# Performance work log

Hardware: AMD Instinct MI355X
Metric: run time of the kernel (lower is better)

## Reference

```python
import jax, jax.numpy as jnp
import numpy as np

K, N, E, D = 4, 2048, 4096, 128
BETA = 0.6
EPS = 0.01           # epsilon in hard-sigmoid gating
LAM = 0.05           # lambda_schedule
TC0, TCMAX = 0.3, 0.7
COS_EPS = 1e-8       # F.cosine_similarity eps
MAX_SCORED_EDGES = 500
EDGE_DENSITY = 0.008


def setup_inputs() -> dict:
    key = jax.random.key(0)
    ks = jax.random.split(key, 8)
    s = 0.02
    H = (jax.random.uniform(ks[0], (K, N, E)) < EDGE_DENSITY).astype(jnp.float32)
    X = jax.random.normal(ks[1], (N, D), jnp.float32)
    return dict(
        H=H, X=X, epoch=50,
        mlp_w1=jax.random.normal(ks[2], (K, D, D), jnp.float32) * s,
        mlp_b1=jnp.zeros((K, D), jnp.float32),
        mlp_w2=jax.random.normal(ks[3], (K, D, D), jnp.float32) * s,
        mlp_b2=jnp.zeros((K, D), jnp.float32),
        comp_W=jax.random.normal(ks[4], (K, D, D), jnp.float32) * 0.01,
        att_w1=jax.random.normal(ks[5], (K, D, D // 2), jnp.float32) * s,
        att_b1=jnp.zeros((K, D // 2), jnp.float32),
        att_w2=jax.random.normal(ks[6], (K, D // 2, 1), jnp.float32) * s,
        att_b2=jnp.zeros((K, 1), jnp.float32),
    )


def reference(H, X, epoch, mlp_w1, mlp_b1, mlp_w2, mlp_b2, comp_W,
              att_w1, att_b1, att_w2, att_b2):
    # ---- component level (Eq. 4, batched over K) ----
    h1 = jax.nn.relu(jnp.einsum('nd,kdh->knh', X, mlp_w1) + mlp_b1[:, None, :])
    Xk = jnp.einsum('knh,khe->kne', h1, mlp_w2) + mlp_b2[:, None, :]        # [K,N,D]
    a1 = jax.nn.relu(jnp.einsum('knd,kdh->knh', Xk, att_w1) + att_b1[:, None, :])
    att = jax.nn.sigmoid(jnp.einsum('knh,kho->kno', a1, att_w2) + att_b2[:, None, :])
    S_att = att.mean(axis=(1, 2))                                            # [K]
    frob = jnp.sqrt((comp_W ** 2).sum(axis=(1, 2)))                          # ||W_k||_F
    featn = jnp.sqrt((Xk ** 2).sum(axis=(1, 2)))                             # ||MLP(X_k)||_2 (Frobenius)
    imp = BETA * frob * featn + (1.0 - BETA) * S_att
    pi_c = jax.nn.softmax(imp)
    theta_c = TC0 + (1.0 - jnp.exp(-LAM * epoch)) * (TCMAX - TC0)            # Eq. 3 schedule
    gates = jnp.clip((pi_c - theta_c) / EPS + 0.5, 0.0, 1.0)                 # hard sigmoid
    # K_min = max(1, int(0.1*K)) = 1 -> force top-1 gate open
    keep = jax.nn.one_hot(jnp.argmax(gates), K, dtype=gates.dtype)
    gates = jnp.maximum(gates, keep)

    xnorm = jnp.linalg.norm(X, axis=1)                                       # [N]
    xhat = X / jnp.maximum(xnorm, COS_EPS)[:, None]
    er = jnp.arange(E)
    eye = jnp.eye(N, dtype=bool)

    Hp_l, eg_l, npi_l = [], [], []
    for k in range(K):  # small fixed component count
        Hk = H[k]
        mask = Hk > 0                                                        # [N,E]
        cnt = mask.sum(axis=0)                                               # nodes per hyperedge
        order = jnp.cumsum(mask, axis=0)
        i = jnp.argmax(mask, axis=0)                                         # first incident node
        j = jnp.argmax(mask & (order == 2), axis=0)                          # second incident node
        cos = (xhat[i] * xhat[j]).sum(-1)                                    # [E]
        A = Hk[i, er] * Hk[j, er]                                            # A_ij per edge
        # torch loop: only first 500 edges scored; <2-node edges get 0.1; rest 0
        imp_e = jnp.where(er < MAX_SCORED_EDGES,
                          jnp.where(cnt >= 2, A * cos, 0.1), 0.0)
        pi_e = jax.nn.softmax(imp_e)
        theta_e = jnp.minimum(theta_c, pi_e.mean() + jnp.std(pi_e, ddof=1))  # torch.std unbiased
        eg = jnp.clip((pi_e - theta_e) / EPS + 0.5, 0.0, 1.0)
        eg = jnp.where((eg.sum() < 1.0) & (er == jnp.argmax(pi_e)), 1.0, eg)
        eg_eff = jnp.where(gates[k] > 0.5, eg, jnp.ones_like(eg))
        Hp = Hk * gates[k] * eg_eff[None, :]                                 # pruned incidence

        # ---- node level (Eq. 7) on pruned graph ----
        B = (Hp > 0).astype(Hk.dtype)
        Adj = ((B @ B.T) > 0) & (~eye)                                       # shared-hyperedge neighbors
        degf = Adj.sum(axis=1).astype(Hk.dtype)
        nsum = Adj.astype(Hk.dtype) @ xhat                                   # sum of neighbor unit vecs
        avg = jnp.where(degf > 0, (xhat * nsum).sum(-1) / jnp.maximum(degf, 1.0), 0.0)
        npi = jax.nn.softmax(avg * xnorm)
        Hp_l.append(Hp); eg_l.append(eg); npi_l.append(npi)

    return (jnp.stack(Hp_l), gates, jnp.stack(eg_l), jnp.stack(npi_l))
```

## Files before the change

kernel.cpp:

```cpp
#include <hip/hip_runtime.h>
#include <math.h>

#define KCOMP 4
#define NN 2048
#define EE 4096
#define DD 128
#define MAXNE 96
#define MAXSE 500
#define BETA_C 0.6f
#define EPS_G 0.01f
#define LAM_S 0.05f
#define TC0_C 0.3f
#define TCMAX_C 0.7f
#define COS_EPS_C 1e-8f

typedef float vf4 __attribute__((ext_vector_type(4)));

static const size_t OFF_XHAT   = 0;
static const size_t OFF_XNORM  = 1048576;
static const size_t OFF_SCAL   = 1056768;
static const size_t OFF_NCNT   = 1057024;
static const size_t OFF_EMASK  = 1089792;
static const size_t OFF_NELIST = 5284096;
static const size_t OFF_IMPE   = 6856960;
static const size_t OFF_EGS    = 6865152;
static const size_t OFF_Z      = 6930688;
static const size_t OFF_FEAT   = 6963456;
static const size_t OFF_ATT    = 6965504;
static const size_t OFF_FROB   = 6967552;

__global__ __launch_bounds__(1024) void k_d1(
    const float4* __restrict__ H4, unsigned* __restrict__ emask,
    const float* __restrict__ X, float* __restrict__ xhat, float* __restrict__ xnorm,
    const float* __restrict__ w1, const float* __restrict__ b1,
    const float* __restrict__ w2, const float* __restrict__ b2,
    const float* __restrict__ aw1, const float* __restrict__ ab1,
    const float* __restrict__ aw2, const float* __restrict__ ab2,
    const float4* __restrict__ compW4,
    float* __restrict__ featA, float* __restrict__ attA, float* __restrict__ frobA) {
  __shared__ char smem[28928];
  int b = blockIdx.x, t = threadIdx.x;
  if (b < 256) {
    unsigned* lds = (unsigned*)smem;
    int k = b >> 6;
    int rem = b & 63;
    int ch_super = rem >> 4;
    int e4_super = rem & 15;
    int chi = t >> 6;
    int e4i = t & 63;
    int ch = ch_super * 16 + chi;
    int e4 = e4_super * 64 + e4i;
    int n0 = ch * 32;
    const float4* p = H4 + ((size_t)(k * NN + n0)) * (EE / 4) + e4;
    unsigned w0 = 0, w1b = 0, w2b = 0, w3 = 0;
    for (int rb = 0; rb < 32; rb += 8) {
      float4 v[8];
#pragma unroll
      for (int u = 0; u < 8; ++u) v[u] = p[(size_t)(rb + u) * (EE / 4)];
#pragma unroll
      for (int u = 0; u < 8; ++u) {
        unsigned bit = 1u << (rb + u);
        w0  |= (v[u].x > 0.f) ? bit : 0u;
        w1b |= (v[u].y > 0.f) ? bit : 0u;
        w2b |= (v[u].z > 0.f) ? bit : 0u;
        w3  |= (v[u].w > 0.f) ? bit : 0u;
      }
    }
    int el = e4i * 4;
    lds[(el + 0) * 17 + chi] = w0;
    lds[(el + 1) * 17 + chi] = w1b;
    lds[(el + 2) * 17 + chi] = w2b;
    lds[(el + 3) * 17 + chi] = w3;
    __syncthreads();
    int e_base = e4_super * 256;
    int wi = t & 15;
    int eo = t >> 4;
#pragma unroll
    for (int it = 0; it < 4; ++it) {
      int e_local = it * 64 + eo;
      emask[((size_t)(k * EE) + e_base + e_local) * 64 + ch_super * 16 + wi] =
          lds[e_local * 17 + wi];
    }
    return;
  }
  if (b < 384) {
    int node = (b - 256) * 16 + (t >> 6);
    int lane = t & 63;
    float2 v = ((const float2*)X)[(size_t)node * 64 + lane];
    float ss = v.x * v.x + v.y * v.y;
    for (int o = 32; o > 0; o >>= 1) ss += __shfl_xor(ss, o, 64);
    float nrm = sqrtf(ss);
    float den = fmaxf(nrm, COS_EPS_C);
    if (lane == 0) xnorm[node] = nrm;
    float2 o2; o2.x = v.x / den; o2.y = v.y / den;
    ((float2*)xhat)[(size_t)node * 64 + lane] = o2;
    return;
  }
  if (b < 896) {
    int mb = b - 384;
    int k = mb >> 7;
    int bx = mb & 127;
    float* Xs  = (float*)smem;
    float* H1s = Xs + 2048;
    float* XKs = H1s + 2048;
    float* A1s = XKs + 2048;
    float* red = A1s + 1024;
    int n0 = bx * 16;
    for (int i = t; i < 16 * 128; i += 1024) Xs[i] = X[(size_t)n0 * 128 + i];
    __syncthreads();

    int h = t & 127, g = t >> 7;
    const float* W1 = w1 + (size_t)k * 128 * 128;
    float acc0 = b1[k * 128 + h], acc1 = acc0;
    for (int d = 0; d < 128; d += 4) {
      float wa = W1[(d + 0) * 128 + h];
      float wb = W1[(d + 1) * 128 + h];
      float wc = W1[(d + 2) * 128 + h];
      float wd = W1[(d + 3) * 128 + h];
      float4 x0 = *(const float4*)&Xs[(g * 2 + 0) * 128 + d];
      float4 x1 = *(const float4*)&Xs[(g * 2 + 1) * 128 + d];
      acc0 = fmaf(x0.x, wa, acc0); acc0 = fmaf(x0.y, wb, acc0);
      acc0 = fmaf(x0.z, wc, acc0); acc0 = fmaf(x0.w, wd, acc0);
      acc1 = fmaf(x1.x, wa, acc1); acc1 = fmaf(x1.y, wb, acc1);
      acc1 = fmaf(x1.z, wc, acc1); acc1 = fmaf(x1.w, wd, acc1);
    }
    H1s[(g * 2 + 0) * 128 + h] = fmaxf(acc0, 0.f);
    H1s[(g * 2 + 1) * 128 + h] = fmaxf(acc1, 0.f);
    __syncthreads();

    const float* W2 = w2 + (size_t)k * 128 * 128;
    acc0 = b2[k * 128 + h]; acc1 = acc0;
    for (int d = 0; d < 128; d += 4) {
      float wa = W2[(d + 0) * 128 + h];
      float wb = W2[(d + 1) * 128 + h];
      float wc = W2[(d + 2) * 128 + h];
      float wd = W2[(d + 3) * 128 + h];
      float4 x0 = *(const float4*)&H1s[(g * 2 + 0) * 128 + d];
      float4 x1 = *(const float4*)&H1s[(g * 2 + 1) * 128 + d];
      acc0 = fmaf(x0.x, wa, acc0); acc0 = fmaf(x0.y, wb, acc0);
      acc0 = fmaf(x0.z, wc, acc0); acc0 = fmaf(x0.w, wd, acc0);
      acc1 = fmaf(x1.x, wa, acc1); acc1 = fmaf(x1.y, wb, acc1);
      acc1 = fmaf(x1.z, wc, acc1); acc1 = fmaf(x1.w, wd, acc1);
    }
    float fpart = fmaf(acc1, acc1, acc0 * acc0);
    XKs[(g * 2 + 0) * 128 + h] = acc0;
    XKs[(g * 2 + 1) * 128 + h] = acc1;
    __syncthreads();

    int h2 = t & 63, g4 = t >> 6;
    const float* AW1 = aw1 + (size_t)k * 128 * 64;
    float a0 = ab1[k * 64 + h2];
    for (int d = 0; d < 128; d += 4) {
      float4 xv = *(const float4*)&XKs[g4 * 128 + d];
      a0 = fmaf(xv.x, AW1[(d + 0) * 64 + h2], a0);
      a0 = fmaf(xv.y, AW1[(d + 1) * 64 + h2], a0);
      a0 = fmaf(xv.z, AW1[(d + 2) * 64 + h2], a0);
      a0 = fmaf(xv.w, AW1[(d + 3) * 64 + h2], a0);
    }
    A1s[g4 * 64 + h2] = fmaxf(a0, 0.f);
    __syncthreads();

    float attsum = 0.f;
    if (t < 16) {
      const float* AW2 = aw2 + (size_t)k * 64;
      float a = ab2[k];
      for (int d = 0; d < 64; d += 4) {
        float4 av = *(const float4*)&A1s[t * 64 + d];
        a = fmaf(av.x, AW2[d + 0], a);
        a = fmaf(av.y, AW2[d + 1], a);
        a = fmaf(av.z, AW2[d + 2], a);
        a = fmaf(av.w, AW2[d + 3], a);
      }
      attsum = 1.f / (1.f + expf(-a));
    }
    for (int o = 32; o > 0; o >>= 1) {
      fpart  += __shfl_xor(fpart, o, 64);
      attsum += __shfl_xor(attsum, o, 64);
    }
    int wv = t >> 6, ln = t & 63;
    if (ln == 0) { red[wv] = fpart; red[16 + wv] = attsum; }
    __syncthreads();
    if (t == 0) {
      float fs = 0.f, as = 0.f;
#pragma unroll
      for (int i = 0; i < 16; i++) { fs += red[i]; as += red[16 + i]; }
      featA[k * 128 + bx] = fs;
      attA[k * 128 + bx]  = as;
    }
    return;
  }
  {
    int fb = b - 896;
    int k = fb >> 2, idx = fb & 3;
    float* red = (float*)smem;
    float4 v = compW4[(size_t)k * 4096 + idx * 1024 + t];
    float s = v.x * v.x + v.y * v.y + v.z * v.z + v.w * v.w;
    for (int o = 32; o > 0; o >>= 1) s += __shfl_xor(s, o, 64);
    int wv = t >> 6, ln = t & 63;
    if (ln == 0) red[wv] = s;
    __syncthreads();
    if (t == 0) {
      float fs = 0.f;
#pragma unroll
      for (int i = 0; i < 16; i++) fs += red[i];
      frobA[k * 4 + idx] = fs;
    }
  }
}

__global__ void k_d2(const unsigned* __restrict__ emask, int* __restrict__ ncnt,
                     unsigned short* __restrict__ nelist, const float* __restrict__ xhat,
                     float* __restrict__ impE) {
  __shared__ char smem[32 * MAXNE * 2 + 128];
  int t = threadIdx.x;
  int k = blockIdx.y;
  int bx = blockIdx.x;
  if (bx < 64) {
    unsigned short* lst = (unsigned short*)smem;
    int* lcnt = (int*)(smem + 32 * MAXNE * 2);
    int w = bx;
    if (t < 32) lcnt[t] = 0;
    __syncthreads();
    for (int e = t; e < EE; e += 256) {
      unsigned wd = emask[((size_t)(k * EE) + e) * 64 + w];
      while (wd) {
        int b2 = __builtin_ctz(wd); wd &= wd - 1;
        int slot = atomicAdd(&lcnt[b2], 1);
        if (slot < MAXNE) lst[b2 * MAXNE + slot] = (unsigned short)e;
      }
    }
    __syncthreads();
    if (t < 32) ncnt[k * NN + w * 32 + t] = lcnt[t];
    for (int i = t; i < 32 * MAXNE; i += 256) {
      int b2 = i / MAXNE, s = i - b2 * MAXNE;
      int c = lcnt[b2]; if (c > MAXNE) c = MAXNE;
      if (s < c) nelist[((size_t)(k * NN + w * 32 + b2)) * MAXNE + s] = lst[b2 * MAXNE + s];
    }
    return;
  }
  int e = (bx - 64) * 4 + (t >> 6);
  int lane = t & 63;
  unsigned w = emask[((size_t)(k * EE) + e) * 64 + lane];
  int pc = __popc(w);
  for (int o = 32; o > 0; o >>= 1) pc += __shfl_xor(pc, o, 64);
  float impv = 0.1f;
  if (pc >= 2) {
    unsigned l1 = w ? (unsigned)((lane << 5) + __builtin_ctz(w)) : 0xffffffffu;
    unsigned wr = w & (w - 1);
    unsigned l2 = wr ? (unsigned)((lane << 5) + __builtin_ctz(wr)) : 0xffffffffu;
    unsigned g1 = l1;
    for (int o = 32; o > 0; o >>= 1) {
      unsigned x = (unsigned)__shfl_xor((int)g1, o, 64);
      g1 = g1 < x ? g1 : x;
    }
    unsigned cand = (l1 == g1) ? l2 : l1;
    unsigned g2 = cand;
    for (int o = 32; o > 0; o >>= 1) {
      unsigned x = (unsigned)__shfl_xor((int)g2, o, 64);
      g2 = g2 < x ? g2 : x;
    }
    float2 xi = ((const float2*)xhat)[(size_t)g1 * 64 + lane];
    float2 xj = ((const float2*)xhat)[(size_t)g2 * 64 + lane];
    float d = xi.x * xj.x + xi.y * xj.y;
    for (int o = 32; o > 0; o >>= 1) d += __shfl_xor(d, o, 64);
    impv = d;
  }
  if (lane == 0) impE[k * 512 + e] = impv;
}

__device__ __forceinline__ float blockReduceSum16(float v, float* red, int t) {
  for (int o = 32; o > 0; o >>= 1) v += __shfl_xor(v, o, 64);
  __syncthreads();
  if ((t & 63) == 0) red[t >> 6] = v;
  __syncthreads();
  float s = red[0];
#pragma unroll
  for (int i = 1; i < 16; i++) s += red[i];
  return s;
}

__global__ void k_edgegate(const float* __restrict__ impE,
                           const float* __restrict__ featA, const float* __restrict__ attA,
                           const float* __restrict__ frobA, float* __restrict__ scal,
                           const int* __restrict__ epoch, float* __restrict__ out_gates,
                           float* __restrict__ egscaled, float* __restrict__ out_eg) {
  __shared__ float red[16];
  __shared__ int redi[16];
  __shared__ float imps[KCOMP];
  int k = blockIdx.x;
  int t = threadIdx.x;
  int wv0 = t >> 6, ln0 = t & 63;
  if (wv0 < KCOMP) {
    float pf = 0.f, pa = 0.f;
    for (int i = ln0; i < 128; i += 64) { pf += featA[wv0 * 128 + i]; pa += attA[wv0 * 128 + i]; }
    float pr = (ln0 < 4) ? frobA[wv0 * 4 + ln0] : 0.f;
    for (int o = 32; o > 0; o >>= 1) {
      pf += __shfl_xor(pf, o, 64);
      pa += __shfl_xor(pa, o, 64);
      pr += __shfl_xor(pr, o, 64);
    }
    if (ln0 == 0)
      imps[wv0] = BETA_C * sqrtf(pr) * sqrtf(pf) + (1.f - BETA_C) * (pa / (float)NN);
  }
  __syncthreads();
  float gates[KCOMP];
  float tc;
  {
    float mx = imps[0];
    for (int kk = 1; kk < KCOMP; kk++) mx = fmaxf(mx, imps[kk]);
    float ex[KCOMP], ssum = 0.f;
    for (int kk = 0; kk < KCOMP; kk++) { ex[kk] = expf(imps[kk] - mx); ssum += ex[kk]; }
    tc = TC0_C + (1.f - expf(-LAM_S * (float)epoch[0])) * (TCMAX_C - TC0_C);
    for (int kk = 0; kk < KCOMP; kk++) {
      float pi = ex[kk] / ssum;
      gates[kk] = fminf(fmaxf((pi - tc) / EPS_G + 0.5f, 0.f), 1.f);
    }
    int am = 0; float bv2 = gates[0];
    for (int kk = 1; kk < KCOMP; kk++) if (gates[kk] > bv2) { bv2 = gates[kk]; am = kk; }
    gates[am] = fmaxf(gates[am], 1.f);
  }
  if (t == 0) {
    scal[12 + k] = gates[k];
    if (k == 0) for (int kk = 0; kk < KCOMP; kk++) out_gates[kk] = gates[kk];
  }
  float imp[4];
#pragma unroll
  for (int j = 0; j < 4; j++) {
    int e = t + j * 1024;
    imp[j] = (e < MAXSE) ? impE[k * 512 + e] : 0.f;
  }
  float m = fmaxf(fmaxf(imp[0], imp[1]), fmaxf(imp[2], imp[3]));
  for (int o = 32; o > 0; o >>= 1) m = fmaxf(m, __shfl_xor(m, o, 64));
  __syncthreads();
  if ((t & 63) == 0) red[t >> 6] = m;
  __syncthreads();
  m = red[0];
#pragma unroll
  for (int i = 1; i < 16; i++) m = fmaxf(m, red[i]);
  float p[4], psum = 0.f;
#pragma unroll
  for (int j = 0; j < 4; j++) { p[j] = expf(imp[j] - m); psum += p[j]; }
  float S = blockReduceSum16(psum, red, t);
  float pi[4], tot = 0.f;
#pragma unroll
  for (int j = 0; j < 4; j++) { pi[j] = p[j] / S; tot += pi[j]; }
  float T = blockReduceSum16(tot, red, t);
  float mean = T / (float)EE;
  float devs = 0.f;
#pragma unroll
  for (int j = 0; j < 4; j++) { float d = pi[j] - mean; devs = fmaf(d, d, devs); }
  float V = blockReduceSum16(devs, red, t);
  float stdv = sqrtf(V / (float)(EE - 1));
  float theta = fminf(tc, mean + stdv);
  float eg[4], egsum = 0.f;
#pragma unroll
  for (int j = 0; j < 4; j++) {
    eg[j] = fminf(fmaxf((pi[j] - theta) / EPS_G + 0.5f, 0.f), 1.f);
    egsum += eg[j];
  }
  float EGS = blockReduceSum16(egsum, red, t);
  float bv = -1e30f; int bi = 0x7fffffff;
#pragma unroll
  for (int j = 0; j < 4; j++) if (pi[j] > bv) { bv = pi[j]; bi = t + j * 1024; }
  for (int o = 32; o > 0; o >>= 1) {
    float ov = __shfl_xor(bv, o, 64); int oi = __shfl_xor(bi, o, 64);
    if (ov > bv || (ov == bv && oi < bi)) { bv = ov; bi = oi; }
  }
  __syncthreads();
  if ((t & 63) == 0) { red[t >> 6] = bv; redi[t >> 6] = bi; }
  __syncthreads();
  float abv = red[0]; int abi = redi[0];
#pragma unroll
  for (int i = 1; i < 16; i++) {
    float ov = red[i]; int oi = redi[i];
    if (ov > abv || (ov == abv && oi < abi)) { abv = ov; abi = oi; }
  }
  float g = gates[k];
#pragma unroll
  for (int j = 0; j < 4; j++) {
    int e = t + j * 1024;
    float egv = eg[j];
    if (EGS < 1.f && e == abi) egv = 1.f;
    out_eg[(size_t)k * EE + e] = egv;
    float eff = (g > 0.5f) ? egv : 1.f;
    egscaled[k * EE + e] = g * eff;
  }
}

__global__ void k_hprow(const unsigned* __restrict__ emask,
                        const int* __restrict__ ncnt, const unsigned short* __restrict__ nelist,
                        const float* __restrict__ egs, const float* __restrict__ scal,
                        const float* __restrict__ xhat, const float* __restrict__ xnorm,
                        float* __restrict__ out, float* __restrict__ z) {
  __shared__ float row[EE];
  __shared__ unsigned short elds[MAXNE];
  __shared__ unsigned wpart[4][64];
  __shared__ unsigned short list[2048];
  __shared__ int cnt_s;
  __shared__ float sred[4];
  int k = blockIdx.y, n = blockIdx.x, t = threadIdx.x;
  float g = scal[12 + k];
  vf4* o4 = (vf4*)(out + ((size_t)(k * NN + n)) * EE);
  if (g <= 0.f) {
    vf4 z4 = {0.f, 0.f, 0.f, 0.f};
#pragma unroll
    for (int i = 0; i < 4; i++) __builtin_nontemporal_store(z4, &o4[t + i * 256]);
    if (t == 0) z[k * NN + n] = 0.f;
    return;
  }
  int ec = ncnt[k * NN + n]; if (ec > MAXNE) ec = MAXNE;
  if (t < ec) elds[t] = nelist[((size_t)(k * NN + n)) * MAXNE + t];
  vf4* row4 = (vf4*)row;
  vf4 z4 = {0.f, 0.f, 0.f, 0.f};
#pragma unroll
  for (int i = 0; i < 4; i++) row4[t + i * 256] = z4;
  if (t == 0) cnt_s = 0;
  __syncthreads();
  if (t < ec) {
    int e = elds[t];
    row[e] = egs[k * EE + e];
  }
  __syncthreads();
#pragma unroll
  for (int i = 0; i < 4; i++) __builtin_nontemporal_store(row4[t + i * 256], &o4[t + i * 256]);
  int lane = t & 63, wv = t >> 6;
  unsigned acc = 0;
  for (int it = wv; it < ec; it += 4) {
    int e = (int)elds[it];
    if (row[e] > 0.f) acc |= emask[((size_t)(k * EE) + e) * 64 + lane];
  }
  wpart[wv][lane] = acc;
  __syncthreads();
  if (t < 64) {
    unsigned w = wpart[0][t] | wpart[1][t] | wpart[2][t] | wpart[3][t];
    if (t == (n >> 5)) w &= ~(1u << (n & 31));
    int c = __popc(w);
    if (c > 0) {
      int base = atomicAdd(&cnt_s, c);
      while (w) {
        int b = __builtin_ctz(w); w &= w - 1;
        list[base++] = (unsigned short)((t << 5) + b);
      }
    }
  }
  __syncthreads();
  int cnt = cnt_s;
  if (cnt == 0) { if (t == 0) z[k * NN + n] = 0.f; return; }
  int fc = lane & 31, hh = lane >> 5;
  float4 xn4 = ((const float4*)xhat)[(size_t)n * 32 + fc];
  float a = 0.f;
#pragma unroll 4
  for (int it = wv * 2 + hh; it < cnt; it += 8) {
    int m = (int)list[it];
    float4 xm = ((const float4*)xhat)[(size_t)m * 32 + fc];
    a += xn4.x * xm.x + xn4.y * xm.y + xn4.z * xm.z + xn4.w * xm.w;
  }
  for (int o = 32; o > 0; o >>= 1) a += __shfl_xor(a, o, 64);
  if (lane == 0) sred[wv] = a;
  __syncthreads();
  if (t == 0) {
    float s = sred[0] + sred[1] + sred[2] + sred[3];
    z[k * NN + n] = (s / (float)cnt) * xnorm[n];
  }
}

__global__ void k_npi(const float* __restrict__ z, float* __restrict__ out_npi) {
  __shared__ float red[4];
  int k = blockIdx.x, t = threadIdx.x;
  float v[8]; float m = -1e30f;
#pragma unroll
  for (int j = 0; j < 8; j++) { v[j] = z[k * NN + t + j * 256]; m = fmaxf(m, v[j]); }
  for (int o = 32; o > 0; o >>= 1) m = fmaxf(m, __shfl_xor(m, o, 64));
  if ((t & 63) == 0) red[t >> 6] = m;
  __syncthreads();
  m = fmaxf(fmaxf(red[0], red[1]), fmaxf(red[2], red[3]));
  __syncthreads();
  float pe[8]; float s = 0.f;
#pragma unroll
  for (int j = 0; j < 8; j++) { pe[j] = expf(v[j] - m); s += pe[j]; }
  for (int o = 32; o > 0; o >>= 1) s += __shfl_xor(s, o, 64);
  if ((t & 63) == 0) red[t >> 6] = s;
  __syncthreads();
  s = red[0] + red[1] + red[2] + red[3];
#pragma unroll
  for (int j = 0; j < 8; j++) out_npi[k * NN + t + j * 256] = pe[j] / s;
}

extern "C" void kernel_launch(void* const* d_in, const int* in_sizes, int n_in,
                              void* d_out, int out_size, void* d_ws, size_t ws_size,
                              hipStream_t stream) {
  const float* H     = (const float*)d_in[0];
  const float* X     = (const float*)d_in[1];
  const int*   epoch = (const int*)d_in[2];
  const float* w1    = (const float*)d_in[3];
  const float* b1    = (const float*)d_in[4];
  const float* w2    = (const float*)d_in[5];
  const float* b2    = (const float*)d_in[6];
  const float* compW = (const float*)d_in[7];
  const float* aw1   = (const float*)d_in[8];
  const float* ab1   = (const float*)d_in[9];
  const float* aw2   = (const float*)d_in[10];
  const float* ab2   = (const float*)d_in[11];

  char* ws = (char*)d_ws;
  float* xhat  = (float*)(ws + OFF_XHAT);
  float* xnorm = (float*)(ws + OFF_XNORM);
  float* scal  = (float*)(ws + OFF_SCAL);
  int*   ncnt  = (int*)(ws + OFF_NCNT);
  unsigned* emask = (unsigned*)(ws + OFF_EMASK);
  unsigned short* nelist = (unsigned short*)(ws + OFF_NELIST);
  float* impE  = (float*)(ws + OFF_IMPE);
  float* egs   = (float*)(ws + OFF_EGS);
  float* zbuf  = (float*)(ws + OFF_Z);
  float* featA = (float*)(ws + OFF_FEAT);
  float* attA  = (float*)(ws + OFF_ATT);
  float* frobA = (float*)(ws + OFF_FROB);

  float* out       = (float*)d_out;
  float* out_gates = out + (size_t)KCOMP * NN * EE;
  float* out_eg    = out_gates + KCOMP;
  float* out_npi   = out_eg + (size_t)KCOMP * EE;

  k_d1<<<912, 1024, 0, stream>>>((const float4*)H, emask, X, xhat, xnorm,
                                 w1, b1, w2, b2, aw1, ab1, aw2, ab2,
                                 (const float4*)compW, featA, attA, frobA);
  k_d2<<<dim3(189, KCOMP), 256, 0, stream>>>(emask, ncnt, nelist, xhat, impE);
  k_edgegate<<<KCOMP, 1024, 0, stream>>>(impE, featA, attA, frobA, scal, epoch,
                                         out_gates, egs, out_eg);
  k_hprow<<<dim3(NN, KCOMP), 256, 0, stream>>>(emask, ncnt, nelist, egs, scal, xhat, xnorm,
                                               out, zbuf);
  k_npi<<<KCOMP, 256, 0, stream>>>(zbuf, out_npi);
}
```

Baseline: 330.9 us.

## Retile MLP blocks to 64 nodes and build node edge lists via global atomics

The component MLP/attention blocks now process 64 nodes each with 8 register accumulators per thread, reusing each weight load across more rows and cutting block count, and are placed first in the fused launch. The node-to-edge list construction switches from per-word shared-memory lists to edge-chunk scans with global atomicAdd on per-node counters, which are zeroed inside the first kernel. This reduces redundant emask reads and grid size but introduces global atomic contention and nondeterministic list order.

```diff
diff --git a/kernel.cpp b/kernel.cpp
--- a/kernel.cpp
+++ b/kernel.cpp
@@ -36,14 +36,131 @@
     const float* __restrict__ w2, const float* __restrict__ b2,
     const float* __restrict__ aw1, const float* __restrict__ ab1,
     const float* __restrict__ aw2, const float* __restrict__ ab2,
-    const float4* __restrict__ compW4,
+    const float4* __restrict__ compW4, int* __restrict__ ncnt,
     float* __restrict__ featA, float* __restrict__ attA, float* __restrict__ frobA) {
-  __shared__ char smem[28928];
+  __shared__ float smem[16416];
   int b = blockIdx.x, t = threadIdx.x;
-  if (b < 256) {
+  if (b < 128) {
+    int k = b >> 5;
+    int bx = b & 31;
+    float* Xs  = smem;
+    float* H1s = smem + 8192;
+    float* A1s = H1s;
+    float* red = smem + 16384;
+    int n0 = bx * 64;
+    for (int i = t; i < 64 * 128; i += 1024) Xs[i] = X[(size_t)n0 * 128 + i];
+    __syncthreads();
+
+    int h = t & 127, g = t >> 7;
+    const float* W1 = w1 + (size_t)k * 128 * 128;
+    float acc[8];
+    {
+      float bb = b1[k * 128 + h];
+#pragma unroll
+      for (int rr = 0; rr < 8; ++rr) acc[rr] = bb;
+    }
+    for (int d = 0; d < 128; d += 4) {
+      float wa = W1[(d + 0) * 128 + h];
+      float wb = W1[(d + 1) * 128 + h];
+      float wc = W1[(d + 2) * 128 + h];
+      float wd2 = W1[(d + 3) * 128 + h];
+#pragma unroll
+      for (int rr = 0; rr < 8; ++rr) {
+        float4 x = *(const float4*)&Xs[(g * 8 + rr) * 128 + d];
+        acc[rr] = fmaf(x.x, wa, acc[rr]); acc[rr] = fmaf(x.y, wb, acc[rr]);
+        acc[rr] = fmaf(x.z, wc, acc[rr]); acc[rr] = fmaf(x.w, wd2, acc[rr]);
+      }
+    }
+#pragma unroll
+    for (int rr = 0; rr < 8; ++rr) H1s[(g * 8 + rr) * 128 + h] = fmaxf(acc[rr], 0.f);
+    __syncthreads();
+
+    const float* W2 = w2 + (size_t)k * 128 * 128;
+    {
+      float bb = b2[k * 128 + h];
+#pragma unroll
+      for (int rr = 0; rr < 8; ++rr) acc[rr] = bb;
+    }
+    for (int d = 0; d < 128; d += 4) {
+      float wa = W2[(d + 0) * 128 + h];
+      float wb = W2[(d + 1) * 128 + h];
+      float wc = W2[(d + 2) * 128 + h];
+      float wd2 = W2[(d + 3) * 128 + h];
+#pragma unroll
+      for (int rr = 0; rr < 8; ++rr) {
+        float4 x = *(const float4*)&H1s[(g * 8 + rr) * 128 + d];
+        acc[rr] = fmaf(x.x, wa, acc[rr]); acc[rr] = fmaf(x.y, wb, acc[rr]);
+        acc[rr] = fmaf(x.z, wc, acc[rr]); acc[rr] = fmaf(x.w, wd2, acc[rr]);
+      }
+    }
+    float fpart = 0.f;
+    __syncthreads();
+#pragma unroll
+    for (int rr = 0; rr < 8; ++rr) {
+      Xs[(g * 8 + rr) * 128 + h] = acc[rr];
+      fpart = fmaf(acc[rr], acc[rr], fpart);
+    }
+    __syncthreads();
+
+    int h2 = t & 63, g4 = t >> 6;
+    const float* AW1 = aw1 + (size_t)k * 128 * 64;
+    float a4[4];
+    {
+      float ab = ab1[k * 64 + h2];
+#pragma unroll
+      for (int q = 0; q < 4; ++q) a4[q] = ab;
+    }
+    for (int d = 0; d < 128; d += 4) {
+      float wa = AW1[(d + 0) * 64 + h2];
+      float wb = AW1[(d + 1) * 64 + h2];
+      float wc = AW1[(d + 2) * 64 + h2];
+      float wd2 = AW1[(d + 3) * 64 + h2];
+#pragma unroll
+      for (int q = 0; q < 4; ++q) {
+        float4 x = *(const float4*)&Xs[(g4 * 4 + q) * 128 + d];
+        a4[q] = fmaf(x.x, wa, a4[q]); a4[q] = fmaf(x.y, wb, a4[q]);
+        a4[q] = fmaf(x.z, wc, a4[q]); a4[q] = fmaf(x.w, wd2, a4[q]);
+      }
+    }
+    __syncthreads();
+#pragma unroll
+    for (int q = 0; q < 4; ++q) A1s[(g4 * 4 + q) * 64 + h2] = fmaxf(a4[q], 0.f);
+    __syncthreads();
+
+    float attsum = 0.f;
+    if (t < 64) {
+      const float* AW2 = aw2 + (size_t)k * 64;
+      float a = ab2[k];
+      for (int d = 0; d < 64; d += 4) {
+        float4 av = *(const float4*)&A1s[t * 64 + d];
+        a = fmaf(av.x, AW2[d + 0], a);
+        a = fmaf(av.y, AW2[d + 1], a);
+        a = fmaf(av.z, AW2[d + 2], a);
+        a = fmaf(av.w, AW2[d + 3], a);
+      }
+      attsum = 1.f / (1.f + expf(-a));
+    }
+    for (int o = 32; o > 0; o >>= 1) {
+      fpart  += __shfl_xor(fpart, o, 64);
+      attsum += __shfl_xor(attsum, o, 64);
+    }
+    int wv = t >> 6, ln = t & 63;
+    if (ln == 0) { red[wv] = fpart; red[16 + wv] = attsum; }
+    __syncthreads();
+    if (t == 0) {
+      float fs = 0.f, as = 0.f;
+#pragma unroll
+      for (int i = 0; i < 16; i++) { fs += red[i]; as += red[16 + i]; }
+      featA[k * 128 + bx] = fs;
+      attA[k * 128 + bx]  = as;
+    }
+    return;
+  }
+  if (b < 384) {
     unsigned* lds = (unsigned*)smem;
-    int k = b >> 6;
-    int rem = b & 63;
+    int sb = b - 128;
+    int k = sb >> 6;
+    int rem = sb & 63;
     int ch_super = rem >> 4;
     int e4_super = rem & 15;
     int chi = t >> 6;
@@ -83,8 +200,10 @@
     }
     return;
   }
-  if (b < 384) {
-    int node = (b - 256) * 16 + (t >> 6);
+  if (b < 512) {
+    int xb = b - 384;
+    if (t < 64) ncnt[xb * 64 + t] = 0;
+    int node = xb * 16 + (t >> 6);
     int lane = t & 63;
     float2 v = ((const float2*)X)[(size_t)node * 64 + lane];
     float ss = v.x * v.x + v.y * v.y;
@@ -96,103 +215,10 @@
     ((float2*)xhat)[(size_t)node * 64 + lane] = o2;
     return;
   }
-  if (b < 896) {
-    int mb = b - 384;
-    int k = mb >> 7;
-    int bx = mb & 127;
-    float* Xs  = (float*)smem;
-    float* H1s = Xs + 2048;
-    float* XKs = H1s + 2048;
-    float* A1s = XKs + 2048;
-    float* red = A1s + 1024;
-    int n0 = bx * 16;
-    for (int i = t; i < 16 * 128; i += 1024) Xs[i] = X[(size_t)n0 * 128 + i];
-    __syncthreads();
-
-    int h = t & 127, g = t >> 7;
-    const float* W1 = w1 + (size_t)k * 128 * 128;
-    float acc0 = b1[k * 128 + h], acc1 = acc0;
-    for (int d = 0; d < 128; d += 4) {
-      float wa = W1[(d + 0) * 128 + h];
-      float wb = W1[(d + 1) * 128 + h];
-      float wc = W1[(d + 2) * 128 + h];
-      float wd = W1[(d + 3) * 128 + h];
-      float4 x0 = *(const float4*)&Xs[(g * 2 + 0) * 128 + d];
-      float4 x1 = *(const float4*)&Xs[(g * 2 + 1) * 128 + d];
-      acc0 = fmaf(x0.x, wa, acc0); acc0 = fmaf(x0.y, wb, acc0);
-      acc0 = fmaf(x0.z, wc, acc0); acc0 = fmaf(x0.w, wd, acc0);
-      acc1 = fmaf(x1.x, wa, acc1); acc1 = fmaf(x1.y, wb, acc1);
-      acc1 = fmaf(x1.z, wc, acc1); acc1 = fmaf(x1.w, wd, acc1);
-    }
-    H1s[(g * 2 + 0) * 128 + h] = fmaxf(acc0, 0.f);
-    H1s[(g * 2 + 1) * 128 + h] = fmaxf(acc1, 0.f);
-    __syncthreads();
-
-    const float* W2 = w2 + (size_t)k * 128 * 128;
-    acc0 = b2[k * 128 + h]; acc1 = acc0;
-    for (int d = 0; d < 128; d += 4) {
-      float wa = W2[(d + 0) * 128 + h];
-      float wb = W2[(d + 1) * 128 + h];
-      float wc = W2[(d + 2) * 128 + h];
-      float wd = W2[(d + 3) * 128 + h];
-      float4 x0 = *(const float4*)&H1s[(g * 2 + 0) * 128 + d];
-      float4 x1 = *(const float4*)&H1s[(g * 2 + 1) * 128 + d];
-      acc0 = fmaf(x0.x, wa, acc0); acc0 = fmaf(x0.y, wb, acc0);
-      acc0 = fmaf(x0.z, wc, acc0); acc0 = fmaf(x0.w, wd, acc0);
-      acc1 = fmaf(x1.x, wa, acc1); acc1 = fmaf(x1.y, wb, acc1);
-      acc1 = fmaf(x1.z, wc, acc1); acc1 = fmaf(x1.w, wd, acc1);
-    }
-    float fpart = fmaf(acc1, acc1, acc0 * acc0);
-    XKs[(g * 2 + 0) * 128 + h] = acc0;
-    XKs[(g * 2 + 1) * 128 + h] = acc1;
-    __syncthreads();
-
-    int h2 = t & 63, g4 = t >> 6;
-    const float* AW1 = aw1 + (size_t)k * 128 * 64;
-    float a0 = ab1[k * 64 + h2];
-    for (int d = 0; d < 128; d += 4) {
-      float4 xv = *(const float4*)&XKs[g4 * 128 + d];
-      a0 = fmaf(xv.x, AW1[(d + 0) * 64 + h2], a0);
-      a0 = fmaf(xv.y, AW1[(d + 1) * 64 + h2], a0);
-      a0 = fmaf(xv.z, AW1[(d + 2) * 64 + h2], a0);
-      a0 = fmaf(xv.w, AW1[(d + 3) * 64 + h2], a0);
-    }
-    A1s[g4 * 64 + h2] = fmaxf(a0, 0.f);
-    __syncthreads();
-
-    float attsum = 0.f;
-    if (t < 16) {
-      const float* AW2 = aw2 + (size_t)k * 64;
-      float a = ab2[k];
-      for (int d = 0; d < 64; d += 4) {
-        float4 av = *(const float4*)&A1s[t * 64 + d];
-        a = fmaf(av.x, AW2[d + 0], a);
-        a = fmaf(av.y, AW2[d + 1], a);
-        a = fmaf(av.z, AW2[d + 2], a);
-        a = fmaf(av.w, AW2[d + 3], a);
-      }
-      attsum = 1.f / (1.f + expf(-a));
-    }
-    for (int o = 32; o > 0; o >>= 1) {
-      fpart  += __shfl_xor(fpart, o, 64);
-      attsum += __shfl_xor(attsum, o, 64);
-    }
-    int wv = t >> 6, ln = t & 63;
-    if (ln == 0) { red[wv] = fpart; red[16 + wv] = attsum; }
-    __syncthreads();
-    if (t == 0) {
-      float fs = 0.f, as = 0.f;
-#pragma unroll
-      for (int i = 0; i < 16; i++) { fs += red[i]; as += red[16 + i]; }
-      featA[k * 128 + bx] = fs;
-      attA[k * 128 + bx]  = as;
-    }
-    return;
-  }
   {
-    int fb = b - 896;
+    int fb = b - 512;
     int k = fb >> 2, idx = fb & 3;
-    float* red = (float*)smem;
+    float* red = smem;
     float4 v = compW4[(size_t)k * 4096 + idx * 1024 + t];
     float s = v.x * v.x + v.y * v.y + v.z * v.z + v.w * v.w;
     for (int o = 32; o > 0; o >>= 1) s += __shfl_xor(s, o, 64);
@@ -211,34 +237,28 @@
 __global__ void k_d2(const unsigned* __restrict__ emask, int* __restrict__ ncnt,
                      unsigned short* __restrict__ nelist, const float* __restrict__ xhat,
                      float* __restrict__ impE) {
-  __shared__ char smem[32 * MAXNE * 2 + 128];
   int t = threadIdx.x;
   int k = blockIdx.y;
   int bx = blockIdx.x;
-  if (bx < 64) {
-    unsigned short* lst = (unsigned short*)smem;
-    int* lcnt = (int*)(smem + 32 * MAXNE * 2);
-    int w = bx;
-    if (t < 32) lcnt[t] = 0;
-    __syncthreads();
-    for (int e = t; e < EE; e += 256) {
-      unsigned wd = emask[((size_t)(k * EE) + e) * 64 + w];
-      while (wd) {
-        int b2 = __builtin_ctz(wd); wd &= wd - 1;
-        int slot = atomicAdd(&lcnt[b2], 1);
-        if (slot < MAXNE) lst[b2 * MAXNE + slot] = (unsigned short)e;
-      }
-    }
-    __syncthreads();
-    if (t < 32) ncnt[k * NN + w * 32 + t] = lcnt[t];
-    for (int i = t; i < 32 * MAXNE; i += 256) {
-      int b2 = i / MAXNE, s = i - b2 * MAXNE;
-      int c = lcnt[b2]; if (c > MAXNE) c = MAXNE;
-      if (s < c) nelist[((size_t)(k * NN + w * 32 + b2)) * MAXNE + s] = lst[b2 * MAXNE + s];
+  if (bx < 16) {
+    const unsigned* base = emask + (size_t)k * EE * 64 + (size_t)bx * 256 * 64;
+    int e0 = bx * 256;
+    for (int i = t; i < 256 * 64; i += 256) {
+      unsigned wdw = base[i];
+      if (!wdw) continue;
+      int e = e0 + (i >> 6);
+      int wrd = i & 63;
+      do {
+        int bit = __builtin_ctz(wdw); wdw &= wdw - 1;
+        int node = wrd * 32 + bit;
+        int slot = atomicAdd(&ncnt[k * NN + node], 1);
+        if (slot < MAXNE)
+          nelist[((size_t)(k * NN + node)) * MAXNE + slot] = (unsigned short)e;
+      } while (wdw);
     }
     return;
   }
-  int e = (bx - 64) * 4 + (t >> 6);
+  int e = (bx - 16) * 4 + (t >> 6);
   int lane = t & 63;
   unsigned w = emask[((size_t)(k * EE) + e) * 64 + lane];
   int pc = __popc(w);
@@ -291,8 +311,8 @@
   int t = threadIdx.x;
   int wv0 = t >> 6, ln0 = t & 63;
   if (wv0 < KCOMP) {
-    float pf = 0.f, pa = 0.f;
-    for (int i = ln0; i < 128; i += 64) { pf += featA[wv0 * 128 + i]; pa += attA[wv0 * 128 + i]; }
+    float pf = (ln0 < 32) ? featA[wv0 * 128 + ln0] : 0.f;
+    float pa = (ln0 < 32) ? attA[wv0 * 128 + ln0] : 0.f;
     float pr = (ln0 < 4) ? frobA[wv0 * 4 + ln0] : 0.f;
     for (int o = 32; o > 0; o >>= 1) {
       pf += __shfl_xor(pf, o, 64);
@@ -521,10 +541,10 @@
   float* out_eg    = out_gates + KCOMP;
   float* out_npi   = out_eg + (size_t)KCOMP * EE;
 
-  k_d1<<<912, 1024, 0, stream>>>((const float4*)H, emask, X, xhat, xnorm,
+  k_d1<<<528, 1024, 0, stream>>>((const float4*)H, emask, X, xhat, xnorm,
                                  w1, b1, w2, b2, aw1, ab1, aw2, ab2,
-                                 (const float4*)compW, featA, attA, frobA);
-  k_d2<<<dim3(189, KCOMP), 256, 0, stream>>>(emask, ncnt, nelist, xhat, impE);
+                                 (const float4*)compW, ncnt, featA, attA, frobA);
+  k_d2<<<dim3(141, KCOMP), 256, 0, stream>>>(emask, ncnt, nelist, xhat, impE);
   k_edgegate<<<KCOMP, 1024, 0, stream>>>(impE, featA, attA, frobA, scal, epoch,
                                          out_gates, egs, out_eg);
   k_hprow<<<dim3(NN, KCOMP), 256, 0, stream>>>(emask, ncnt, nelist, egs, scal, xhat, xnorm,
```

Measured after the change: 372.5 us. +12.6%, slower.
